# Kernel optimization log

Measured on AMD Instinct MI355X. Metric: run time of the kernel, lower is better.

## Reference

```python
import jax, jax.numpy as jnp
import numpy as np

B, C, T = 2, 128, 25000
OUT_C = 128
N_NODES = B * T            # 50000, nodes after flatten
N_EDGES = 800000           # avg degree 16


def setup_inputs() -> dict:
    key = jax.random.key(0)
    k1, k2, k3 = jax.random.split(key, 3)
    x = jax.random.normal(k1, (B, C, T), dtype=jnp.float32)
    W = jax.random.normal(k2, (C, OUT_C), dtype=jnp.float32) * (1.0 / np.sqrt(C))
    bias = jnp.zeros((OUT_C,), dtype=jnp.float32)
    edge_index = jax.random.randint(k3, (2, N_EDGES), 0, N_NODES, dtype=jnp.int64)
    return {"x": x, "W": W, "bias": bias, "edge_index": edge_index}


def reference(x, W, bias, edge_index):
    b, c, t = x.shape
    n = b * t
    flat = x.transpose(0, 2, 1).reshape(n, c)          # [N, C]
    h = flat @ W                                       # [N, OUT_C] transform first (GCNConv)
    src, dst = edge_index[0], edge_index[1]
    # in-degree with self-loops (PyG GCNConv default symmetric norm)
    deg = jnp.zeros((n,), dtype=h.dtype).at[dst].add(1.0) + 1.0
    dinv_sqrt = jax.lax.rsqrt(deg)
    norm = dinv_sqrt[src] * dinv_sqrt[dst]             # [E]
    msgs = h[src] * norm[:, None]                      # [E, OUT_C] gather + scale
    agg = jax.ops.segment_sum(msgs, dst, num_segments=n)
    agg = agg + h * (1.0 / deg)[:, None]               # self-loop term: norm_ii = 1/deg_i
    out = jax.nn.relu(agg + bias)
    return out.reshape(b, t, -1).transpose(0, 2, 1)    # [B, OUT_C, T]
```

## Files before the change

### kernel.cpp

```cpp
#include <hip/hip_runtime.h>

#define TT 25000
#define BB 2
#define CC 128
#define NN (BB*TT)
#define NB ((NN + 255) / 256)

typedef __attribute__((ext_vector_type(8))) short bf16x8;
typedef __attribute__((ext_vector_type(4))) float f32x4;

__device__ inline unsigned short f2bf(float f) {
    unsigned int u = __float_as_uint(f);
    u += 0x7FFF + ((u >> 16) & 1);
    return (unsigned short)(u >> 16);
}
__device__ inline float bfhi(unsigned int v) { return __uint_as_float(v << 16); }
__device__ inline float bflo(unsigned int v) { return __uint_as_float(v & 0xFFFF0000u); }

__global__ __launch_bounds__(256) void k_deg(const int* __restrict__ dst, int E,
                                             int* __restrict__ deg,
                                             int* __restrict__ eseq) {
    int base = blockIdx.x * 1024 + threadIdx.x;
    int d[4]; bool ok[4];
#pragma unroll
    for (int u = 0; u < 4; ++u) {
        int i = base + u * 256;
        ok[u] = (i < E);
        d[u] = ok[u] ? dst[i] : 0;
    }
#pragma unroll
    for (int u = 0; u < 4; ++u)
        if (ok[u]) eseq[base + u * 256] = atomicAdd(&deg[d[u]], 1);
}

__global__ __launch_bounds__(256) void k_bsum(const int* __restrict__ deg,
                                              int* __restrict__ bsum) {
    __shared__ int red[256];
    int tid = threadIdx.x;
    int i = blockIdx.x * 256 + tid;
    red[tid] = (i < NN) ? deg[i] : 0;
    __syncthreads();
#pragma unroll
    for (int o = 128; o > 0; o >>= 1) {
        if (tid < o) red[tid] += red[tid + o];
        __syncthreads();
    }
    if (tid == 0) bsum[blockIdx.x] = red[0];
}

__global__ __launch_bounds__(256) void k_scan2(const int* __restrict__ deg,
                                               const int* __restrict__ bsum,
                                               int* __restrict__ off,
                                               float* __restrict__ dinv) {
    __shared__ int part[256];
    __shared__ int bpref;
    int tid = threadIdx.x;
    int i = blockIdx.x * 256 + tid;

    part[tid] = (tid < NB && tid < blockIdx.x) ? bsum[tid] : 0;
    __syncthreads();
#pragma unroll
    for (int o = 128; o > 0; o >>= 1) {
        if (tid < o) part[tid] += part[tid + o];
        __syncthreads();
    }
    if (tid == 0) bpref = part[0];
    __syncthreads();
    int base = bpref;
    __syncthreads();

    int v = (i < NN) ? deg[i] : 0;
    part[tid] = v;
    __syncthreads();
#pragma unroll
    for (int o = 1; o < 256; o <<= 1) {
        int u = (tid >= o) ? part[tid - o] : 0;
        __syncthreads();
        part[tid] += u;
        __syncthreads();
    }
    int incl = part[tid];
    if (i < NN) {
        off[i]  = base + incl - v;
        dinv[i] = rsqrtf((float)(v + 1));
    }
    if (i == NN - 1) off[NN] = base + incl;
}

__global__ __launch_bounds__(256) void k_fill(const int* __restrict__ src,
                                              const int* __restrict__ dst, int E,
                                              const int* __restrict__ off,
                                              const int* __restrict__ eseq,
                                              int* __restrict__ csr_src) {
    int i = blockIdx.x * blockDim.x + threadIdx.x;
    if (i < E) {
        int d = dst[i];
        csr_src[off[d] + eseq[i]] = src[i];
    }
}

__global__ __launch_bounds__(256) void k_gemm(const float* __restrict__ x,
                                              const float* __restrict__ W,
                                              const float* __restrict__ dinv,
                                              unsigned short* __restrict__ h) {
    __shared__ __align__(16) unsigned short a_lds[4][4][64][8];
    __shared__ __align__(16) unsigned short b_lds[8][4][64][8];
    int tid = threadIdx.x;
    int n0 = blockIdx.x * 64;

    {
        int m = tid & 63;
        int n = n0 + m;
        bool ok = (n < NN);
        int b = 0, t = 0;
        if (ok) { b = n / TT; t = n - b * TT; }
        const float* xp = x + ((size_t)b * CC) * TT + t;
        int mt = m >> 4, lm = m & 15;
#pragma unroll
        for (int p = 0; p < 4; ++p) {
            int kg = (tid >> 6) + p * 4;
            unsigned short tmp[8];
#pragma unroll
            for (int j = 0; j < 8; ++j) {
                float v = ok ? xp[(size_t)(kg * 8 + j) * TT] : 0.f;
                tmp[j] = f2bf(v);
            }
            int kk = kg >> 2, q = kg & 3;
            *(bf16x8*)&a_lds[mt][kk][lm | (q << 4)][0] = *(bf16x8*)tmp;
        }
    }
    {
        int nc = tid & 127;
        int nt = nc >> 4, ln = nc & 15;
#pragma unroll
        for (int p = 0; p < 8; ++p) {
            int kg = (tid >> 7) + p * 2;
            unsigned short tmp[8];
#pragma unroll
            for (int j = 0; j < 8; ++j)
                tmp[j] = f2bf(W[(kg * 8 + j) * CC + nc]);
            int kk = kg >> 2, q = kg & 3;
            *(bf16x8*)&b_lds[nt][kk][ln | (q << 4)][0] = *(bf16x8*)tmp;
        }
    }
    __syncthreads();

    int lane = tid & 63;
    int w = tid >> 6;
    f32x4 acc[8];
#pragma unroll
    for (int nt = 0; nt < 8; ++nt) acc[nt] = (f32x4){0.f, 0.f, 0.f, 0.f};
#pragma unroll
    for (int kk = 0; kk < 4; ++kk) {
        bf16x8 a = *(const bf16x8*)&a_lds[w][kk][lane][0];
#pragma unroll
        for (int nt = 0; nt < 8; ++nt) {
            bf16x8 bb = *(const bf16x8*)&b_lds[nt][kk][lane][0];
            acc[nt] = __builtin_amdgcn_mfma_f32_16x16x32_bf16(a, bb, acc[nt], 0, 0, 0);
        }
    }

    int q = lane >> 4, col = lane & 15;
    int nodebase = n0 + w * 16 + q * 4;
    float di[4];
#pragma unroll
    for (int r = 0; r < 4; ++r) {
        int nn = nodebase + r;
        di[r] = (nn < NN) ? dinv[nn] : 0.f;
    }
#pragma unroll
    for (int nt = 0; nt < 8; ++nt) {
#pragma unroll
        for (int r = 0; r < 4; ++r) {
            int nn = nodebase + r;
            if (nn < NN)
                h[(size_t)nn * CC + nt * 16 + col] = f2bf(di[r] * acc[nt][r]);
        }
    }
}

__global__ __launch_bounds__(256) void k_agg(const unsigned int* __restrict__ hb,
                                             const int* __restrict__ off,
                                             const int* __restrict__ csr_src,
                                             const float* __restrict__ dinv,
                                             const float* __restrict__ bias,
                                             unsigned int* __restrict__ agg16) {
    int lane = threadIdx.x & 63;
    int w    = threadIdx.x >> 6;
    int n    = blockIdx.x * 4 + w;
    if (n >= NN) return;
    float ax = 0.f, ay = 0.f;
    int e0 = off[n], e1 = off[n + 1];

    for (int c0 = e0; c0 < e1; c0 += 64) {
        int cnt = e1 - c0; if (cnt > 64) cnt = 64;
        int li = lane < cnt ? lane : cnt - 1;
        int iv = csr_src[c0 + li];
        int j = 0;
        for (; j + 16 <= cnt; j += 16) {
            int s[16];
#pragma unroll
            for (int u = 0; u < 16; ++u) s[u] = __shfl(iv, j + u, 64);
            unsigned int v[16];
#pragma unroll
            for (int u = 0; u < 16; ++u) v[u] = hb[(size_t)s[u] * 64 + lane];
#pragma unroll
            for (int u = 0; u < 16; ++u) { ax += bfhi(v[u]); ay += bflo(v[u]); }
        }
        for (; j + 4 <= cnt; j += 4) {
            int s[4];
#pragma unroll
            for (int u = 0; u < 4; ++u) s[u] = __shfl(iv, j + u, 64);
            unsigned int v[4];
#pragma unroll
            for (int u = 0; u < 4; ++u) v[u] = hb[(size_t)s[u] * 64 + lane];
#pragma unroll
            for (int u = 0; u < 4; ++u) { ax += bfhi(v[u]); ay += bflo(v[u]); }
        }
        for (; j < cnt; ++j) {
            int s = __shfl(iv, j, 64);
            unsigned int v = hb[(size_t)s * 64 + lane];
            ax += bfhi(v); ay += bflo(v);
        }
    }

    unsigned int hv = hb[(size_t)n * 64 + lane];
    ax += bfhi(hv);
    ay += bflo(hv);
    float di = dinv[n];
    const float2* b2 = (const float2*)bias;
    float2 bb = b2[lane];
    float rx = fmaxf(fmaf(di, ax, bb.x), 0.f);
    float ry = fmaxf(fmaf(di, ay, bb.y), 0.f);
    unsigned int packed = (unsigned int)f2bf(rx) | ((unsigned int)f2bf(ry) << 16);
    agg16[(size_t)n * 64 + lane] = packed;
}

__global__ void k_trans(const unsigned int* __restrict__ agg16, float* __restrict__ out) {
    __shared__ float tile[32][65];
    int t0 = blockIdx.x * 32;
    int p0 = blockIdx.y * 32;
    int b  = blockIdx.z;
    int tx = threadIdx.x, ty = threadIdx.y;
#pragma unroll
    for (int i = 0; i < 4; ++i) {
        int t = t0 + ty + i * 8;
        if (t < TT) {
            unsigned int u = agg16[(size_t)(b * TT + t) * 64 + p0 + tx];
            tile[ty + i * 8][2 * tx]     = bfhi(u);
            tile[ty + i * 8][2 * tx + 1] = bflo(u);
        }
    }
    __syncthreads();
    int t = t0 + tx;
    if (t < TT) {
#pragma unroll
        for (int i = 0; i < 8; ++i) {
            int ch = ty + i * 8;
            out[((size_t)b * CC + 2 * p0 + ch) * TT + t] = tile[tx][ch];
        }
    }
}

extern "C" void kernel_launch(void* const* d_in, const int* in_sizes, int n_in,
                              void* d_out, int out_size, void* d_ws, size_t ws_size,
                              hipStream_t stream) {
    const float* x    = (const float*)d_in[0];
    const float* W    = (const float*)d_in[1];
    const float* bias = (const float*)d_in[2];
    const int*   ei   = (const int*)d_in[3];
    int E = in_sizes[3] / 2;
    const int* src = ei;
    const int* dst = ei + E;
    float* out = (float*)d_out;

    char* ws = (char*)d_ws;
    size_t o = 0;
    unsigned short* h = (unsigned short*)(ws + o); o += (size_t)NN * CC * 2;
    unsigned int* agg16 = (unsigned int*)(ws + o); o += (size_t)NN * 64 * 4;
    int*   deg  = (int*)  (ws + o); o += (size_t)NN * 4;
    float* dinv = (float*)(ws + o); o += (size_t)NN * 4;
    int*   off  = (int*)  (ws + o); o += (size_t)(NN + 1) * 4 + 12;
    int*   bsum = (int*)  (ws + o); o += (size_t)((NB + 3) & ~3) * 4;
    int*   eseq = (int*)  (ws + o); o += (size_t)E * 4;
    int*   csrs = (int*)  (ws + o); o += (size_t)E * 4;

    hipMemsetAsync(deg, 0, (size_t)NN * 4, stream);

    k_deg  <<<(E + 1023) / 1024, 256, 0, stream>>>(dst, E, deg, eseq);
    k_bsum <<<NB, 256, 0, stream>>>(deg, bsum);
    k_scan2<<<NB, 256, 0, stream>>>(deg, bsum, off, dinv);
    k_fill <<<(E + 255) / 256, 256, 0, stream>>>(src, dst, E, off, eseq, csrs);
    k_gemm <<<(NN + 63) / 64, 256, 0, stream>>>(x, W, dinv, h);
    k_agg  <<<(NN + 3) / 4, 256, 0, stream>>>((const unsigned int*)h, off, csrs, dinv, bias, agg16);
    dim3 tg((TT + 31) / 32, 2, BB);
    k_trans<<<tg, dim3(32, 8), 0, stream>>>(agg16, out);
}
```

Before: 192.9 us.

## Fuse block-sum into degree count, CSR fill into GEMM, transpose into aggregation

```diff
diff --git a/kernel.cpp b/kernel.cpp
--- a/kernel.cpp
+++ b/kernel.cpp
@@ -5,6 +5,8 @@
 #define CC 128
 #define NN (BB*TT)
 #define NB ((NN + 255) / 256)
+#define NBPAD 256
+#define GEMMB ((NN + 63) / 64)
 
 typedef __attribute__((ext_vector_type(8))) short bf16x8;
 typedef __attribute__((ext_vector_type(4))) float f32x4;
@@ -19,7 +21,12 @@
 
 __global__ __launch_bounds__(256) void k_deg(const int* __restrict__ dst, int E,
                                              int* __restrict__ deg,
-                                             int* __restrict__ eseq) {
+                                             int* __restrict__ eseq,
+                                             int* __restrict__ bsum) {
+    __shared__ int hist[NB];
+    for (int i = threadIdx.x; i < NB; i += 256) hist[i] = 0;
+    __syncthreads();
+
     int base = blockIdx.x * 1024 + threadIdx.x;
     int d[4]; bool ok[4];
 #pragma unroll
@@ -30,22 +37,15 @@
     }
 #pragma unroll
     for (int u = 0; u < 4; ++u)
-        if (ok[u]) eseq[base + u * 256] = atomicAdd(&deg[d[u]], 1);
-}
-
-__global__ __launch_bounds__(256) void k_bsum(const int* __restrict__ deg,
-                                              int* __restrict__ bsum) {
-    __shared__ int red[256];
-    int tid = threadIdx.x;
-    int i = blockIdx.x * 256 + tid;
-    red[tid] = (i < NN) ? deg[i] : 0;
-    __syncthreads();
-#pragma unroll
-    for (int o = 128; o > 0; o >>= 1) {
-        if (tid < o) red[tid] += red[tid + o];
-        __syncthreads();
-    }
-    if (tid == 0) bsum[blockIdx.x] = red[0];
+        if (ok[u]) {
+            eseq[base + u * 256] = atomicAdd(&deg[d[u]], 1);
+            atomicAdd(&hist[d[u] >> 8], 1);
+        }
+    __syncthreads();
+    for (int i = threadIdx.x; i < NB; i += 256) {
+        int v = hist[i];
+        if (v) atomicAdd(&bsum[i], v);
+    }
 }
 
 __global__ __launch_bounds__(256) void k_scan2(const int* __restrict__ deg,
@@ -87,26 +87,29 @@
     if (i == NN - 1) off[NN] = base + incl;
 }
 
-__global__ __launch_bounds__(256) void k_fill(const int* __restrict__ src,
-                                              const int* __restrict__ dst, int E,
-                                              const int* __restrict__ off,
-                                              const int* __restrict__ eseq,
-                                              int* __restrict__ csr_src) {
-    int i = blockIdx.x * blockDim.x + threadIdx.x;
-    if (i < E) {
-        int d = dst[i];
-        csr_src[off[d] + eseq[i]] = src[i];
-    }
-}
-
-__global__ __launch_bounds__(256) void k_gemm(const float* __restrict__ x,
-                                              const float* __restrict__ W,
-                                              const float* __restrict__ dinv,
-                                              unsigned short* __restrict__ h) {
+__global__ __launch_bounds__(256) void k_fg(const float* __restrict__ x,
+                                            const float* __restrict__ W,
+                                            const float* __restrict__ dinv,
+                                            unsigned short* __restrict__ h,
+                                            const int* __restrict__ src,
+                                            const int* __restrict__ dst, int E,
+                                            const int* __restrict__ off,
+                                            const int* __restrict__ eseq,
+                                            int* __restrict__ csr_src) {
     __shared__ __align__(16) unsigned short a_lds[4][4][64][8];
     __shared__ __align__(16) unsigned short b_lds[8][4][64][8];
+    int bx = blockIdx.x;
+    if (bx >= GEMMB) {
+        int i = (bx - GEMMB) * 256 + threadIdx.x;
+        if (i < E) {
+            int d = dst[i];
+            csr_src[off[d] + eseq[i]] = src[i];
+        }
+        return;
+    }
+
     int tid = threadIdx.x;
-    int n0 = blockIdx.x * 64;
+    int n0 = bx * 64;
 
     {
         int m = tid & 63;
@@ -179,85 +182,79 @@
     }
 }
 
-__global__ __launch_bounds__(256) void k_agg(const unsigned int* __restrict__ hb,
-                                             const int* __restrict__ off,
-                                             const int* __restrict__ csr_src,
-                                             const float* __restrict__ dinv,
-                                             const float* __restrict__ bias,
-                                             unsigned int* __restrict__ agg16) {
+__global__ __launch_bounds__(512) void k_aggt(const unsigned int* __restrict__ hb,
+                                              const int* __restrict__ off,
+                                              const int* __restrict__ csr_src,
+                                              const float* __restrict__ dinv,
+                                              const float* __restrict__ bias,
+                                              float* __restrict__ out) {
+    __shared__ float tile[32][129];
     int lane = threadIdx.x & 63;
     int w    = threadIdx.x >> 6;
-    int n    = blockIdx.x * 4 + w;
-    if (n >= NN) return;
-    float ax = 0.f, ay = 0.f;
-    int e0 = off[n], e1 = off[n + 1];
-
-    for (int c0 = e0; c0 < e1; c0 += 64) {
-        int cnt = e1 - c0; if (cnt > 64) cnt = 64;
-        int li = lane < cnt ? lane : cnt - 1;
-        int iv = csr_src[c0 + li];
-        int j = 0;
-        for (; j + 16 <= cnt; j += 16) {
-            int s[16];
-#pragma unroll
-            for (int u = 0; u < 16; ++u) s[u] = __shfl(iv, j + u, 64);
-            unsigned int v[16];
-#pragma unroll
-            for (int u = 0; u < 16; ++u) v[u] = hb[(size_t)s[u] * 64 + lane];
-#pragma unroll
-            for (int u = 0; u < 16; ++u) { ax += bfhi(v[u]); ay += bflo(v[u]); }
-        }
-        for (; j + 4 <= cnt; j += 4) {
-            int s[4];
-#pragma unroll
-            for (int u = 0; u < 4; ++u) s[u] = __shfl(iv, j + u, 64);
-            unsigned int v[4];
-#pragma unroll
-            for (int u = 0; u < 4; ++u) v[u] = hb[(size_t)s[u] * 64 + lane];
-#pragma unroll
-            for (int u = 0; u < 4; ++u) { ax += bfhi(v[u]); ay += bflo(v[u]); }
-        }
-        for (; j < cnt; ++j) {
-            int s = __shfl(iv, j, 64);
-            unsigned int v = hb[(size_t)s * 64 + lane];
-            ax += bfhi(v); ay += bflo(v);
-        }
-    }
-
-    unsigned int hv = hb[(size_t)n * 64 + lane];
-    ax += bfhi(hv);
-    ay += bflo(hv);
-    float di = dinv[n];
-    const float2* b2 = (const float2*)bias;
-    float2 bb = b2[lane];
-    float rx = fmaxf(fmaf(di, ax, bb.x), 0.f);
-    float ry = fmaxf(fmaf(di, ay, bb.y), 0.f);
-    unsigned int packed = (unsigned int)f2bf(rx) | ((unsigned int)f2bf(ry) << 16);
-    agg16[(size_t)n * 64 + lane] = packed;
-}
-
-__global__ void k_trans(const unsigned int* __restrict__ agg16, float* __restrict__ out) {
-    __shared__ float tile[32][65];
-    int t0 = blockIdx.x * 32;
-    int p0 = blockIdx.y * 32;
-    int b  = blockIdx.z;
-    int tx = threadIdx.x, ty = threadIdx.y;
-#pragma unroll
-    for (int i = 0; i < 4; ++i) {
-        int t = t0 + ty + i * 8;
-        if (t < TT) {
-            unsigned int u = agg16[(size_t)(b * TT + t) * 64 + p0 + tx];
-            tile[ty + i * 8][2 * tx]     = bfhi(u);
-            tile[ty + i * 8][2 * tx + 1] = bflo(u);
-        }
-    }
-    __syncthreads();
-    int t = t0 + tx;
-    if (t < TT) {
+    int n0   = blockIdx.x * 32;
+    const float2 bb = ((const float2*)bias)[lane];
+
+#pragma unroll
+    for (int r = 0; r < 4; ++r) {
+        int lt = w * 4 + r;
+        int n = n0 + lt;
+        if (n < NN) {
+            float ax = 0.f, ay = 0.f;
+            int e0 = off[n], e1 = off[n + 1];
+
+            for (int c0 = e0; c0 < e1; c0 += 64) {
+                int cnt = e1 - c0; if (cnt > 64) cnt = 64;
+                int li = lane < cnt ? lane : cnt - 1;
+                int iv = csr_src[c0 + li];
+                int j = 0;
+                for (; j + 16 <= cnt; j += 16) {
+                    int s[16];
+#pragma unroll
+                    for (int u = 0; u < 16; ++u) s[u] = __shfl(iv, j + u, 64);
+                    unsigned int v[16];
+#pragma unroll
+                    for (int u = 0; u < 16; ++u) v[u] = hb[(size_t)s[u] * 64 + lane];
+#pragma unroll
+                    for (int u = 0; u < 16; ++u) { ax += bfhi(v[u]); ay += bflo(v[u]); }
+                }
+                for (; j + 4 <= cnt; j += 4) {
+                    int s[4];
+#pragma unroll
+                    for (int u = 0; u < 4; ++u) s[u] = __shfl(iv, j + u, 64);
+                    unsigned int v[4];
+#pragma unroll
+                    for (int u = 0; u < 4; ++u) v[u] = hb[(size_t)s[u] * 64 + lane];
+#pragma unroll
+                    for (int u = 0; u < 4; ++u) { ax += bfhi(v[u]); ay += bflo(v[u]); }
+                }
+                for (; j < cnt; ++j) {
+                    int s = __shfl(iv, j, 64);
+                    unsigned int v = hb[(size_t)s * 64 + lane];
+                    ax += bfhi(v); ay += bflo(v);
+                }
+            }
+
+            unsigned int hv = hb[(size_t)n * 64 + lane];
+            ax += bfhi(hv);
+            ay += bflo(hv);
+            float di = dinv[n];
+            float rx = fmaxf(fmaf(di, ax, bb.x), 0.f);
+            float ry = fmaxf(fmaf(di, ay, bb.y), 0.f);
+            tile[lt][2 * lane]     = rx;
+            tile[lt][2 * lane + 1] = ry;
+        }
+    }
+    __syncthreads();
+
+    int tx = threadIdx.x & 31;
+    int cg = threadIdx.x >> 5;
+    int n = n0 + tx;
+    if (n < NN) {
+        int b = n / TT, t = n - b * TT;
 #pragma unroll
         for (int i = 0; i < 8; ++i) {
-            int ch = ty + i * 8;
-            out[((size_t)b * CC + 2 * p0 + ch) * TT + t] = tile[tx][ch];
+            int ch = cg + i * 16;
+            out[((size_t)b * CC + ch) * TT + t] = tile[tx][ch];
         }
     }
 }
@@ -277,22 +274,18 @@
     char* ws = (char*)d_ws;
     size_t o = 0;
     unsigned short* h = (unsigned short*)(ws + o); o += (size_t)NN * CC * 2;
-    unsigned int* agg16 = (unsigned int*)(ws + o); o += (size_t)NN * 64 * 4;
     int*   deg  = (int*)  (ws + o); o += (size_t)NN * 4;
+    int*   bsum = (int*)  (ws + o); o += (size_t)NBPAD * 4;
     float* dinv = (float*)(ws + o); o += (size_t)NN * 4;
     int*   off  = (int*)  (ws + o); o += (size_t)(NN + 1) * 4 + 12;
-    int*   bsum = (int*)  (ws + o); o += (size_t)((NB + 3) & ~3) * 4;
     int*   eseq = (int*)  (ws + o); o += (size_t)E * 4;
     int*   csrs = (int*)  (ws + o); o += (size_t)E * 4;
 
-    hipMemsetAsync(deg, 0, (size_t)NN * 4, stream);
-
-    k_deg  <<<(E + 1023) / 1024, 256, 0, stream>>>(dst, E, deg, eseq);
-    k_bsum <<<NB, 256, 0, stream>>>(deg, bsum);
+    hipMemsetAsync(deg, 0, (size_t)(NN + NBPAD) * 4, stream);
+
+    int fb = (E + 255) / 256;
+    k_deg  <<<(E + 1023) / 1024, 256, 0, stream>>>(dst, E, deg, eseq, bsum);
     k_scan2<<<NB, 256, 0, stream>>>(deg, bsum, off, dinv);
-    k_fill <<<(E + 255) / 256, 256, 0, stream>>>(src, dst, E, off, eseq, csrs);
-    k_gemm <<<(NN + 63) / 64, 256, 0, stream>>>(x, W, dinv, h);
-    k_agg  <<<(NN + 3) / 4, 256, 0, stream>>>((const unsigned int*)h, off, csrs, dinv, bias, agg16);
-    dim3 tg((TT + 31) / 32, 2, BB);
-    k_trans<<<tg, dim3(32, 8), 0, stream>>>(agg16, out);
-}
+    k_fg   <<<GEMMB + fb, 256, 0, stream>>>(x, W, dinv, h, src, dst, E, off, eseq, csrs);
+    k_aggt <<<(NN + 31) / 32, 512, 0, stream>>>((const unsigned int*)h, off, csrs, dinv, bias, out);
+}
```

New measurement: 195.6 us. About the same (+1.4%).
